# Kernel optimization log

Hardware: AMD Instinct MI355X
Metric: run time of the kernel (lower is better)

## Reference

```python
import jax, jax.numpy as jnp
import numpy as np
import math

B, S, D, H = 4, 1024, 1024, 16
DK = D // H


def setup_inputs() -> dict:
    key = jax.random.key(0)
    ks = jax.random.split(key, 13)
    s = 1.0 / math.sqrt(D)
    inp = {
        "query": jax.random.normal(ks[0], (B, S, D), jnp.float32),
        "key": jax.random.normal(ks[1], (B, S, D), jnp.float32),
        "value": jax.random.normal(ks[2], (B, S, D), jnp.float32),
        "mask": jax.random.randint(ks[3], (B, S, S), 0, 2, jnp.int32),
        "wq": jax.random.normal(ks[4], (D, D), jnp.float32) * s,
        "bq": jax.random.normal(ks[5], (D,), jnp.float32) * s,
        "wk": jax.random.normal(ks[6], (D, D), jnp.float32) * s,
        "bk": jax.random.normal(ks[7], (D,), jnp.float32) * s,
        "wv": jax.random.normal(ks[8], (D, D), jnp.float32) * s,
        "bv": jax.random.normal(ks[9], (D,), jnp.float32) * s,
        "wo": jax.random.normal(ks[10], (D, D), jnp.float32) * s,
        "bo": jax.random.normal(ks[11], (D,), jnp.float32) * s,
    }
    return inp


def reference(query, key, value, mask, wq, bq, wk, bk, wv, bv, wo, bo):
    # QKV projections, split into heads: [B,S,D] -> [B,H,S,DK]
    def proj(x, w, b):
        return (x @ w.T + b).reshape(B, S, H, DK).transpose(0, 2, 1, 3)

    q = proj(query, wq, bq)
    k = proj(key, wk, bk)
    v = proj(value, wv, bv)

    scores = jnp.einsum("bhqd,bhkd->bhqk", q, k) / math.sqrt(DK)
    scores = scores + mask[:, None, :, :].astype(scores.dtype) * (-1e9)
    p = jax.nn.softmax(scores, axis=-1)
    x = jnp.einsum("bhqk,bhkd->bhqd", p, v)
    x = x.transpose(0, 2, 1, 3).reshape(B, S, D)
    # output projection (dropout is identity in eval)
    return x @ wo.T + bo
```

## Files before the change

### kernel.cpp

```cpp
#include <hip/hip_runtime.h>
#include <hip/hip_bf16.h>


typedef __bf16 bf16x8 __attribute__((ext_vector_type(8)));
typedef float f32x4 __attribute__((ext_vector_type(4)));
typedef unsigned short us8 __attribute__((ext_vector_type(8)));
typedef unsigned short us4 __attribute__((ext_vector_type(4)));

#define MFMA(a, b, c) __builtin_amdgcn_mfma_f32_16x16x32_bf16(a, b, c, 0, 0, 0)
#define EXP2(x) __builtin_amdgcn_exp2f(x)

__device__ __forceinline__ unsigned short f2b(float f) {
  return __builtin_bit_cast(unsigned short, __float2bfloat16(f));
}
__device__ __forceinline__ unsigned cvtpk(float lo, float hi) {
  unsigned r;
  asm("v_cvt_pk_bf16_f32 %0, %1, %2" : "=v"(r) : "v"(lo), "v"(hi));
  return r;
}
__device__ __forceinline__ bf16x8 ldbf8(const unsigned short* p) {
  return __builtin_bit_cast(bf16x8, *reinterpret_cast<const us8*>(p));
}
__device__ __forceinline__ us8 cvt8(float4 a, float4 b) {
  us8 o;
  o[0] = f2b(a.x); o[1] = f2b(a.y); o[2] = f2b(a.z); o[3] = f2b(a.w);
  o[4] = f2b(b.x); o[5] = f2b(b.y); o[6] = f2b(b.z); o[7] = f2b(b.w);
  return o;
}
__device__ __forceinline__ void glds16(const void* g, void* l) {
  __builtin_amdgcn_global_load_lds(
      (const __attribute__((address_space(1))) unsigned int*)g,
      (__attribute__((address_space(3))) unsigned int*)l, 16, 0, 0);
}

__global__ __launch_bounds__(256)
void prep(const float* __restrict__ query, const float* __restrict__ key,
          const float* __restrict__ value, const float* __restrict__ wq,
          const float* __restrict__ wk, const float* __restrict__ wv,
          unsigned short* __restrict__ Abfq, unsigned short* __restrict__ Abfk,
          unsigned short* __restrict__ Abfv, unsigned short* __restrict__ Wb) {
  const int bid = blockIdx.x, tid = threadIdx.x;
  const float* src;
  unsigned short* dst;
  size_t off;
  if (bid < 1536) {
    const int widx = bid >> 9;
    src = (widx == 0) ? wq : (widx == 1) ? wk : wv;
    dst = Wb + (size_t)widx * 1048576;
    off = (size_t)(bid & 511) * 2048 + tid * 8;
  } else if (bid < 3584) {
    src = query; dst = Abfq; off = (size_t)(bid - 1536) * 2048 + tid * 8;
  } else if (bid < 5632) {
    src = key; dst = Abfk; off = (size_t)(bid - 3584) * 2048 + tid * 8;
  } else {
    src = value; dst = Abfv; off = (size_t)(bid - 5632) * 2048 + tid * 8;
  }
  const float4* p = reinterpret_cast<const float4*>(src + off);
  *reinterpret_cast<us8*>(dst + off) = cvt8(p[0], p[1]);
}

__global__ __launch_bounds__(256)
void maskcvt(const int* __restrict__ mask, unsigned char* __restrict__ Mf8) {
  const int idx = blockIdx.x * 256 + threadIdx.x;
  const int wl = idx & 63, tile = idx >> 6;
  const int kt = tile & 63, qt = (tile >> 6) & 63, b = tile >> 12;
  const int lr = wl & 15, lg = wl >> 4;
  const int4 mv = *reinterpret_cast<const int4*>(
      mask + (size_t)(b * 1024 + qt * 16 + lr) * 1024 + kt * 16 + lg * 4);
  uchar4 o;
  o.x = (unsigned char)(mv.x != 0);
  o.y = (unsigned char)(mv.y != 0);
  o.z = (unsigned char)(mv.z != 0);
  o.w = (unsigned char)(mv.w != 0);
  *reinterpret_cast<uchar4*>(Mf8 + (size_t)idx * 4) = o;
}

__global__ __launch_bounds__(512, 6)
void gemm_proj(const unsigned short* __restrict__ Aq,
               const unsigned short* __restrict__ Ak,
               const unsigned short* __restrict__ Av_bf,
               const float* __restrict__ Av_f32,
               const unsigned short* __restrict__ Wb,
               const float* __restrict__ bq, const float* __restrict__ bk,
               const float* __restrict__ bv, unsigned short* __restrict__ Qb,
               unsigned short* __restrict__ Kf, unsigned short* __restrict__ Vf,
               float qscale) {
  constexpr int K = 1024, N = 1024;
  __shared__ __align__(16) unsigned short As[3][128 * 32];
  __shared__ __align__(16) unsigned short Bs[3][128 * 32];
  const int lid = blockIdx.x + (blockIdx.y << 5) + (blockIdx.z << 8);
  const int xcd = lid & 7, slot = lid >> 3;
  const int chunk = ((slot >> 3) << 3) + xcd;
  const int z = chunk >> 5;
  const int bm = (chunk & 31) * 128;
  const int bn = (slot & 7) * 128;

  const unsigned short* Abf = (z == 0) ? Aq : (z == 1) ? Ak : Av_bf;
  const bool f32path = (z == 2) && (Av_bf == nullptr);
  const unsigned short* Bw = Wb + (size_t)z * 1048576;
  const float* bias = (z == 0) ? bq : (z == 1) ? bk : bv;
  const int t = threadIdx.x;
  const int w = t >> 6, lane = t & 63, lr = lane & 15, lg = lane >> 4;
  const int wr = w >> 2, wc = w & 3;

  const int sline = t >> 3;
  const int su = (t & 7) ^ (sline & 7);
  const int srow = sline * 2 + (su >> 2);
  const int scol = (su & 3) * 8;

  f32x4 acc[4][2];
#pragma unroll
  for (int m = 0; m < 4; ++m)
#pragma unroll
    for (int n = 0; n < 2; ++n) acc[m][n] = f32x4{0.f, 0.f, 0.f, 0.f};

  auto stageA = [&](int k0, int buf) {
    const char* g = (const char*)(Abf + (size_t)(bm + srow) * 1024 + k0 + scol);
    char* l = (char*)&As[buf][0] + (w * 64) * 16;
    glds16(g, l);
  };
  auto stageB = [&](int k0, int buf) {
    const char* g = (const char*)(Bw + (size_t)(bn + srow) * 1024 + k0 + scol);
    char* l = (char*)&Bs[buf][0] + (w * 64) * 16;
    glds16(g, l);
  };
#define STA8(buf, v)                                                           \
  { *reinterpret_cast<us8*>((char*)&As[buf][0] + t * 16) = (v); }
#define RDOFF(row) (((row) >> 1) * 128 +                                       \
                    (((lg | (((row) & 1) << 2)) ^ (((row) >> 1) & 7)) * 16))
#define COMPUTE(buf)                                                           \
  {                                                                            \
    bf16x8 af[4], bfr[2];                                                      \
    _Pragma("unroll") for (int m = 0; m < 4; ++m) {                            \
      const int row = wr * 64 + m * 16 + lr;                                   \
      af[m] = ldbf8((const unsigned short*)((char*)&As[buf][0] + RDOFF(row))); \
    }                                                                          \
    _Pragma("unroll") for (int n = 0; n < 2; ++n) {                            \
      const int row = wc * 32 + n * 16 + lr;                                   \
      bfr[n] = ldbf8((const unsigned short*)((char*)&Bs[buf][0] + RDOFF(row)));\
    }                                                                          \
    _Pragma("unroll") for (int m = 0; m < 4; ++m)                              \
        _Pragma("unroll") for (int n = 0; n < 2; ++n)                          \
        acc[m][n] = MFMA(af[m], bfr[n], acc[m][n]);                            \
  }

  if (!f32path) {
    stageA(0, 0);
    stageB(0, 0);
    stageA(32, 1);
    stageB(32, 1);
    for (int c = 0; c < 32; ++c) {
      const int buf = c % 3;
      if (c < 31) {
        asm volatile("s_waitcnt vmcnt(2)" ::: "memory");
      } else {
        asm volatile("s_waitcnt vmcnt(0)" ::: "memory");
      }
      __builtin_amdgcn_s_barrier();
      if (c < 30) {
        const int nb = (c + 2) % 3;
        stageA((c + 2) * 32, nb);
        stageB((c + 2) * 32, nb);
      }
      COMPUTE(buf)
    }
  } else {
    {
      const float4* p =
          reinterpret_cast<const float4*>(Av_f32 + (size_t)(bm + srow) * K + scol);
      STA8(0, cvt8(p[0], p[1]));
      stageB(0, 0);
    }
    __syncthreads();
    for (int c = 0; c < 32; ++c) {
      const int buf = c & 1;
      float4 fa[2];
      if (c < 31) {
        const int k1 = (c + 1) * 32;
        const float4* p = reinterpret_cast<const float4*>(
            Av_f32 + (size_t)(bm + srow) * K + k1 + scol);
        fa[0] = p[0];
        fa[1] = p[1];
        stageB(k1, buf ^ 1);
      }
      COMPUTE(buf)
      if (c < 31) {
        STA8(buf ^ 1, cvt8(fa[0], fa[1]));
      }
      __syncthreads();
    }
  }
#undef STA8
#undef RDOFF
#undef COMPUTE

#pragma unroll
  for (int m = 0; m < 4; ++m) {
    const int mr = bm + wr * 64 + m * 16 + lg * 4;
#pragma unroll
    for (int nt = 0; nt < 2; ++nt) {
      const int n = bn + wc * 32 + nt * 16 + lr;
      const float bb = bias[n];
      if (z == 0) {
#pragma unroll
        for (int r = 0; r < 4; ++r)
          Qb[(size_t)(mr + r) * N + n] = f2b((acc[m][nt][r] + bb) * qscale);
      } else if (z == 1) {
        const int b2 = mr >> 10, s0 = mr & 1023, hh = n >> 6, dd = n & 63;
        const size_t base = (size_t)(b2 * 16 + hh) * 65536 + (size_t)(dd >> 5) * 32768 +
                            (size_t)(s0 >> 4) * 512 +
                            (size_t)((s0 & 15) | (((dd >> 3) & 3) << 4)) * 8 + (dd & 7);
#pragma unroll
        for (int r = 0; r < 4; ++r) Kf[base + r * 8] = f2b(acc[m][nt][r] + bb);
      } else {
        const int b2 = mr >> 10, s0 = mr & 1023, hh = n >> 6, dd = n & 63;
        const size_t base = (size_t)(b2 * 16 + hh) * 65536 + (size_t)(s0 >> 5) * 2048 +
                            (size_t)(dd >> 4) * 512 +
                            (size_t)((dd & 15) | (((s0 >> 3) & 3) << 4)) * 8 + (s0 & 7);
        us4 pk;
#pragma unroll
        for (int r = 0; r < 4; ++r) pk[r] = f2b(acc[m][nt][r] + bb);
        *reinterpret_cast<us4*>(&Vf[base]) = pk;
      }
    }
  }
}

__global__ __launch_bounds__(512, 4)
void gemm_out(const unsigned short* __restrict__ A, const float* __restrict__ Bwf,
              const float* __restrict__ bias, float* __restrict__ Out) {
  constexpr int K = 1024, N = 1024;
  __shared__ __align__(16) unsigned short As[2][128 * 64];
  __shared__ __align__(16) unsigned short Bs[2][64 * 64];
  const int lid = blockIdx.x + (blockIdx.y << 5);
  const int xcd = lid & 7, slot = lid >> 3;
  const int chunk = ((slot >> 5) << 3) + xcd;
  const int pos = slot & 31;
  const int bm = ((chunk << 1) + (pos >> 4)) * 128;
  const int bn = (pos & 15) * 64;
  const int t = threadIdx.x;
  const int w = t >> 6, lane = t & 63, lr = lane & 15, lg = lane >> 4;
  const int wr = w >> 1, wc = w & 1;
  const int swzc = (lr & 7) << 4;
  const int brow = t >> 3, bcol = (t & 7) * 8, bcb = (t & 7) * 16;

  f32x4 acc[2][2];
#pragma unroll
  for (int m = 0; m < 2; ++m)
#pragma unroll
    for (int n = 0; n < 2; ++n) acc[m][n] = f32x4{0.f, 0.f, 0.f, 0.f};

  auto stageA = [&](int k0, int buf) {
#pragma unroll
    for (int it = 0; it < 2; ++it) {
      const int s = it * 512 + t, row = s >> 3, cb = (s & 7) * 16;
      const char* g = (const char*)A + ((size_t)(bm + row) * 1024 + k0) * 2 +
                      (cb ^ ((row & 7) << 4));
      char* l = (char*)&As[buf][0] + (it * 512 + w * 64) * 16;
      glds16(g, l);
    }
  };
  float4 fb[2];
  auto loadB = [&](int k0) {
    const float4* p =
        reinterpret_cast<const float4*>(Bwf + (size_t)(bn + brow) * 1024 + k0 + bcol);
    fb[0] = p[0];
    fb[1] = p[1];
  };
  auto writeB = [&](int buf) {
    *reinterpret_cast<us8*>((char*)&Bs[buf][0] + brow * 128 +
                            (bcb ^ ((brow & 7) << 4))) = cvt8(fb[0], fb[1]);
  };

  stageA(0, 0);
  loadB(0);
  writeB(0);
  __syncthreads();

  for (int c = 0; c < 16; ++c) {
    const int buf = c & 1;
    if (c < 15) {
      const int k1 = (c + 1) * 64;
      stageA(k1, buf ^ 1);
      loadB(k1);
    }
#pragma unroll
    for (int h2 = 0; h2 < 2; ++h2) {
      bf16x8 af[2], bfr[2];
#pragma unroll
      for (int m = 0; m < 2; ++m) {
        const int row = wr * 32 + m * 16 + lr;
        af[m] = ldbf8((const unsigned short*)((char*)&As[buf][0] + row * 128 +
                                              ((h2 * 64 + lg * 16) ^ swzc)));
      }
#pragma unroll
      for (int n = 0; n < 2; ++n) {
        const int row = wc * 32 + n * 16 + lr;
        bfr[n] = ldbf8((const unsigned short*)((char*)&Bs[buf][0] + row * 128 +
                                               ((h2 * 64 + lg * 16) ^ swzc)));
      }
#pragma unroll
      for (int m = 0; m < 2; ++m)
#pragma unroll
        for (int n = 0; n < 2; ++n) acc[m][n] = MFMA(af[m], bfr[n], acc[m][n]);
    }
    if (c < 15) writeB(buf ^ 1);
    __syncthreads();
  }

#pragma unroll
  for (int m = 0; m < 2; ++m) {
    const int mr = bm + wr * 32 + m * 16 + lg * 4;
#pragma unroll
    for (int nt = 0; nt < 2; ++nt) {
      const int n = bn + wc * 32 + nt * 16 + lr;
      const float bb = bias[n];
#pragma unroll
      for (int r = 0; r < 4; ++r) Out[(size_t)(mr + r) * N + n] = acc[m][nt][r] + bb;
    }
  }
}

__global__ __launch_bounds__(256)
void attn_v12(const unsigned short* __restrict__ Qb,
              const unsigned short* __restrict__ Kf,
              const unsigned short* __restrict__ Vf,
              const unsigned char* __restrict__ Mf8,
              unsigned short* __restrict__ ctx) {
  __shared__ __align__(16) unsigned short S[2][8192];
  __shared__ __align__(16) unsigned short sP[4][16 * 64];
  const int lid = blockIdx.x + (blockIdx.y << 6);
  const int xcd = lid & 7, slot = lid >> 3;
  const int bh = ((slot >> 4) << 3) + xcd;
  const int qb = slot & 15;
  const int b = bh >> 4, h = bh & 15;
  const int t = threadIdx.x, w = t >> 6, wl = t & 63, lr = wl & 15, lg = wl >> 4;
  const int q0 = qb * 64 + w * 16;
  const int swz = (lr & 7) << 4;

  const unsigned short* qp = Qb + (size_t)(b * 1024 + q0 + lr) * 1024 + h * 64 + lg * 8;
  const bf16x8 bq0 = ldbf8(qp);
  const bf16x8 bq1 = ldbf8(qp + 32);

  const unsigned short* KfB = Kf + (size_t)bh * 65536;
  const unsigned short* VfB = Vf + (size_t)bh * 65536;
  const unsigned char* mfp = Mf8 + (size_t)((b * 64 + qb * 4 + w) * 64) * 256 + wl * 4;

  f32x4 O[4];
  float l_ = 0.f;
#pragma unroll
  for (int dt = 0; dt < 4; ++dt) O[dt] = f32x4{0.f, 0.f, 0.f, 0.f};
  unsigned short* sp = &sP[w][0];

  auto stage = [&](int kc, int buf) {
    const unsigned short* srcs[4] = {KfB + kc * 2048, KfB + 32768 + kc * 2048,
                                     VfB + kc * 4096, VfB + kc * 4096 + 2048};
#pragma unroll
    for (int r = 0; r < 4; ++r) {
      const char* g = (const char*)(srcs[r] + (size_t)t * 8);
      char* l = (char*)&S[buf][r * 2048 + w * 512];
      glds16(g, l);
    }
  };

  stage(0, 0);
  __syncthreads();

  for (int kc = 0; kc < 16; ++kc) {
    const int buf = kc & 1;
    if (kc < 15) stage(kc + 1, buf ^ 1);

    uchar4 mk[4];
#pragma unroll
    for (int t4 = 0; t4 < 4; ++t4)
      mk[t4] = *reinterpret_cast<const uchar4*>(mfp + (size_t)(kc * 4 + t4) * 256);

    bf16x8 ak[4][2];
#pragma unroll
    for (int t4 = 0; t4 < 4; ++t4) {
      ak[t4][0] = ldbf8(&S[buf][t4 * 512 + wl * 8]);
      ak[t4][1] = ldbf8(&S[buf][2048 + t4 * 512 + wl * 8]);
    }

    f32x4 sc[4];
    __builtin_amdgcn_s_setprio(1);
#pragma unroll
    for (int t4 = 0; t4 < 4; ++t4) {
      f32x4 a;
      a[0] = mk[t4].x ? -1.4427e9f : -24.f;
      a[1] = mk[t4].y ? -1.4427e9f : -24.f;
      a[2] = mk[t4].z ? -1.4427e9f : -24.f;
      a[3] = mk[t4].w ? -1.4427e9f : -24.f;
      a = MFMA(ak[t4][0], bq0, a);
      a = MFMA(ak[t4][1], bq1, a);
      sc[t4] = a;
    }
    __builtin_amdgcn_s_setprio(0);

#pragma unroll
    for (int t4 = 0; t4 < 4; ++t4) {
      const float e0 = EXP2(sc[t4][0]), e1 = EXP2(sc[t4][1]);
      const float e2 = EXP2(sc[t4][2]), e3 = EXP2(sc[t4][3]);
      l_ += (e0 + e1) + (e2 + e3);
      uint2 pw;
      pw.x = cvtpk(e0, e1);
      pw.y = cvtpk(e2, e3);
      *reinterpret_cast<uint2*>((char*)sp + lr * 128 + ((t4 * 32 + lg * 8) ^ swz)) = pw;
    }

    __builtin_amdgcn_s_setprio(1);
#pragma unroll
    for (int ks = 0; ks < 2; ++ks) {
      bf16x8 ap =
          ldbf8((const unsigned short*)((char*)sp + lr * 128 + ((ks * 64 + lg * 16) ^ swz)));
#pragma unroll
      for (int dt = 0; dt < 4; ++dt) {
        bf16x8 bv = ldbf8(&S[buf][4096 + ks * 2048 + dt * 512 + wl * 8]);
        O[dt] = MFMA(ap, bv, O[dt]);
      }
    }
    __builtin_amdgcn_s_setprio(0);

    __syncthreads();
  }

  l_ += __shfl_xor(l_, 16);
  l_ += __shfl_xor(l_, 32);

  float linv[4];
#pragma unroll
  for (int r = 0; r < 4; ++r) linv[r] = 1.0f / __shfl(l_, lg * 4 + r);
#pragma unroll
  for (int dt = 0; dt < 4; ++dt)
#pragma unroll
    for (int r = 0; r < 4; ++r)
      ctx[(size_t)(b * 1024 + q0 + lg * 4 + r) * 1024 + h * 64 + dt * 16 + lr] =
          f2b(O[dt][r] * linv[r]);
}

extern "C" void kernel_launch(void* const* d_in, const int* in_sizes, int n_in,
                              void* d_out, int out_size, void* d_ws, size_t ws_size,
                              hipStream_t stream) {
  const float* query = (const float*)d_in[0];
  const float* key   = (const float*)d_in[1];
  const float* value = (const float*)d_in[2];
  const int*   mask  = (const int*)d_in[3];
  const float* wq = (const float*)d_in[4];
  const float* bq = (const float*)d_in[5];
  const float* wk = (const float*)d_in[6];
  const float* bk = (const float*)d_in[7];
  const float* wv = (const float*)d_in[8];
  const float* bv = (const float*)d_in[9];
  const float* wo = (const float*)d_in[10];
  const float* bo = (const float*)d_in[11];
  float* out = (float*)d_out;

  const size_t SZ = (size_t)4096 * 1024;
  unsigned short* Qb   = (unsigned short*)d_ws;
  unsigned short* Kf   = Qb + SZ;
  unsigned short* Vf   = Kf + SZ;
  unsigned short* ctx  = Vf + SZ;
  unsigned short* Abfq = (unsigned short*)d_out;
  unsigned short* Wb   = Abfq + SZ;
  unsigned char*  Mf8  = (unsigned char*)d_out;
  unsigned short* Abfk = ctx;
  const bool big = ws_size >= (size_t)40 * 1024 * 1024;
  unsigned short* Abfv = big ? (ctx + SZ) : nullptr;

  const float qscale = 0.125f * 1.4426950408889634f;
  dim3 blk(256);
  prep<<<big ? 7680 : 5632, blk, 0, stream>>>(query, key, value, wq, wk, wv,
                                              Abfq, Abfk, Abfv, Wb);
  gemm_proj<<<dim3(32, 8, 3), dim3(512), 0, stream>>>(Abfq, Abfk, Abfv, value, Wb,
                                                      bq, bk, bv, Qb, Kf, Vf, qscale);
  maskcvt<<<4096, blk, 0, stream>>>(mask, Mf8);
  attn_v12<<<dim3(64, 16), blk, 0, stream>>>(Qb, Kf, Vf, Mf8, ctx);
  gemm_out<<<dim3(32, 16), dim3(512), 0, stream>>>(ctx, wo, bo, out);
}
```

Baseline: 112.4 us.

## Pack mask into 16-bit bitfields and fold mask conversion into prep kernel

```diff
diff --git a/kernel.cpp b/kernel.cpp
--- a/kernel.cpp
+++ b/kernel.cpp
@@ -37,9 +37,28 @@
 void prep(const float* __restrict__ query, const float* __restrict__ key,
           const float* __restrict__ value, const float* __restrict__ wq,
           const float* __restrict__ wk, const float* __restrict__ wv,
+          const int* __restrict__ mask,
           unsigned short* __restrict__ Abfq, unsigned short* __restrict__ Abfk,
-          unsigned short* __restrict__ Abfv, unsigned short* __restrict__ Wb) {
+          unsigned short* __restrict__ Abfv, unsigned short* __restrict__ Wb,
+          unsigned short* __restrict__ Mfb, int nconv) {
   const int bid = blockIdx.x, tid = threadIdx.x;
+  if (bid >= nconv) {
+    const int mt = (bid - nconv) * 4 + (tid >> 6);
+    const int wl = tid & 63, lr = wl & 15, lg = wl >> 4;
+    const int kc = mt & 15, qt = (mt >> 4) & 63, b = mt >> 10;
+    const int* mrow = mask + (size_t)(b * 1024 + qt * 16 + lr) * 1024 + kc * 64 + lg * 4;
+    unsigned bits = 0;
+#pragma unroll
+    for (int t4 = 0; t4 < 4; ++t4) {
+      const int4 mv = *reinterpret_cast<const int4*>(mrow + t4 * 16);
+      bits |= (mv.x != 0 ? 1u : 0u) << (t4 * 4 + 0);
+      bits |= (mv.y != 0 ? 1u : 0u) << (t4 * 4 + 1);
+      bits |= (mv.z != 0 ? 1u : 0u) << (t4 * 4 + 2);
+      bits |= (mv.w != 0 ? 1u : 0u) << (t4 * 4 + 3);
+    }
+    Mfb[(size_t)mt * 64 + wl] = (unsigned short)bits;
+    return;
+  }
   const float* src;
   unsigned short* dst;
   size_t off;
@@ -57,22 +76,6 @@
   }
   const float4* p = reinterpret_cast<const float4*>(src + off);
   *reinterpret_cast<us8*>(dst + off) = cvt8(p[0], p[1]);
-}
-
-__global__ __launch_bounds__(256)
-void maskcvt(const int* __restrict__ mask, unsigned char* __restrict__ Mf8) {
-  const int idx = blockIdx.x * 256 + threadIdx.x;
-  const int wl = idx & 63, tile = idx >> 6;
-  const int kt = tile & 63, qt = (tile >> 6) & 63, b = tile >> 12;
-  const int lr = wl & 15, lg = wl >> 4;
-  const int4 mv = *reinterpret_cast<const int4*>(
-      mask + (size_t)(b * 1024 + qt * 16 + lr) * 1024 + kt * 16 + lg * 4);
-  uchar4 o;
-  o.x = (unsigned char)(mv.x != 0);
-  o.y = (unsigned char)(mv.y != 0);
-  o.z = (unsigned char)(mv.z != 0);
-  o.w = (unsigned char)(mv.w != 0);
-  *reinterpret_cast<uchar4*>(Mf8 + (size_t)idx * 4) = o;
 }
 
 __global__ __launch_bounds__(512, 6)
@@ -322,10 +325,10 @@
 }
 
 __global__ __launch_bounds__(256)
-void attn_v12(const unsigned short* __restrict__ Qb,
+void attn_v13(const unsigned short* __restrict__ Qb,
               const unsigned short* __restrict__ Kf,
               const unsigned short* __restrict__ Vf,
-              const unsigned char* __restrict__ Mf8,
+              const unsigned short* __restrict__ Mfb,
               unsigned short* __restrict__ ctx) {
   __shared__ __align__(16) unsigned short S[2][8192];
   __shared__ __align__(16) unsigned short sP[4][16 * 64];
@@ -344,7 +347,7 @@
 
   const unsigned short* KfB = Kf + (size_t)bh * 65536;
   const unsigned short* VfB = Vf + (size_t)bh * 65536;
-  const unsigned char* mfp = Mf8 + (size_t)((b * 64 + qb * 4 + w) * 64) * 256 + wl * 4;
+  const unsigned short* mfp = Mfb + (size_t)((b * 64 + qb * 4 + w) * 16) * 64 + wl;
 
   f32x4 O[4];
   float l_ = 0.f;
@@ -370,10 +373,7 @@
     const int buf = kc & 1;
     if (kc < 15) stage(kc + 1, buf ^ 1);
 
-    uchar4 mk[4];
-#pragma unroll
-    for (int t4 = 0; t4 < 4; ++t4)
-      mk[t4] = *reinterpret_cast<const uchar4*>(mfp + (size_t)(kc * 4 + t4) * 256);
+    const unsigned bits = mfp[kc * 64];
 
     bf16x8 ak[4][2];
 #pragma unroll
@@ -387,10 +387,9 @@
 #pragma unroll
     for (int t4 = 0; t4 < 4; ++t4) {
       f32x4 a;
-      a[0] = mk[t4].x ? -1.4427e9f : -24.f;
-      a[1] = mk[t4].y ? -1.4427e9f : -24.f;
-      a[2] = mk[t4].z ? -1.4427e9f : -24.f;
-      a[3] = mk[t4].w ? -1.4427e9f : -24.f;
+#pragma unroll
+      for (int r = 0; r < 4; ++r)
+        a[r] = (bits >> (t4 * 4 + r)) & 1u ? -1.4427e9f : -24.f;
       a = MFMA(ak[t4][0], bq0, a);
       a = MFMA(ak[t4][1], bq1, a);
       sc[t4] = a;
@@ -462,18 +461,18 @@
   unsigned short* ctx  = Vf + SZ;
   unsigned short* Abfq = (unsigned short*)d_out;
   unsigned short* Wb   = Abfq + SZ;
-  unsigned char*  Mf8  = (unsigned char*)d_out;
+  unsigned short* Mfb  = (unsigned short*)((char*)d_out + (size_t)14 * 1024 * 1024);
   unsigned short* Abfk = ctx;
   const bool big = ws_size >= (size_t)40 * 1024 * 1024;
   unsigned short* Abfv = big ? (ctx + SZ) : nullptr;
+  const int nconv = big ? 7680 : 5632;
 
   const float qscale = 0.125f * 1.4426950408889634f;
   dim3 blk(256);
-  prep<<<big ? 7680 : 5632, blk, 0, stream>>>(query, key, value, wq, wk, wv,
-                                              Abfq, Abfk, Abfv, Wb);
+  prep<<<nconv + 1024, blk, 0, stream>>>(query, key, value, wq, wk, wv, mask,
+                                         Abfq, Abfk, Abfv, Wb, Mfb, nconv);
   gemm_proj<<<dim3(32, 8, 3), dim3(512), 0, stream>>>(Abfq, Abfk, Abfv, value, Wb,
                                                       bq, bk, bv, Qb, Kf, Vf, qscale);
-  maskcvt<<<4096, blk, 0, stream>>>(mask, Mf8);
-  attn_v12<<<dim3(64, 16), blk, 0, stream>>>(Qb, Kf, Vf, Mf8, ctx);
+  attn_v13<<<dim3(64, 16), blk, 0, stream>>>(Qb, Kf, Vf, Mfb, ctx);
   gemm_out<<<dim3(32, 16), dim3(512), 0, stream>>>(ctx, wo, bo, out);
 }
```

New measurement: 111.2 us. Within noise of the previous version (-1.1%).
